# Kernel optimization log

Measured on AMD Instinct MI355X. Metric: run time of the kernel, lower is better.

The kernel has to match this reference:

```python
import jax, jax.numpy as jnp
import numpy as np

N, E = 50000, 800000
IN_CH, OUT_CH, HEADS = 128, 64, 4
NEG_SLOPE = 0.2
BN_EPS = 1e-5


def setup_inputs() -> dict:
    key = jax.random.key(0)
    ks = jax.random.split(key, 8)
    x = jax.random.normal(ks[0], (N, IN_CH), dtype=jnp.float32)
    edge_index = jax.random.randint(ks[1], (2, E), 0, N, dtype=jnp.int64)
    # GATConv params (concat=False: W projects to H*C, output averaged over heads)
    W = jax.random.normal(ks[2], (IN_CH, HEADS * OUT_CH), dtype=jnp.float32) * (1.0 / np.sqrt(IN_CH))
    att_src = jax.random.normal(ks[3], (HEADS, OUT_CH), dtype=jnp.float32) * 0.1
    att_dst = jax.random.normal(ks[4], (HEADS, OUT_CH), dtype=jnp.float32) * 0.1
    bias = jnp.zeros((OUT_CH,), dtype=jnp.float32)
    bn_weight = jnp.ones((OUT_CH,), dtype=jnp.float32)
    bn_bias = jnp.zeros((OUT_CH,), dtype=jnp.float32)
    return {"x": x, "edge_index": edge_index, "W": W, "att_src": att_src,
            "att_dst": att_dst, "bias": bias, "bn_weight": bn_weight, "bn_bias": bn_bias}


def reference(x, edge_index, W, att_src, att_dst, bias, bn_weight, bn_bias):
    # dropout p=0.3 on input and attention weights: identity in eval mode
    n = x.shape[0]
    x_proj = (x @ W).reshape(n, HEADS, OUT_CH)              # [N, H, C]
    a_src = jnp.einsum('nhc,hc->nh', x_proj, att_src)       # [N, H]
    a_dst = jnp.einsum('nhc,hc->nh', x_proj, att_dst)       # [N, H]

    # PyG default add_self_loops=True
    loops = jnp.arange(n, dtype=edge_index.dtype)
    src = jnp.concatenate([edge_index[0], loops])           # [E+N]
    dst = jnp.concatenate([edge_index[1], loops])           # [E+N]

    e = jax.nn.leaky_relu(a_src[src] + a_dst[dst], NEG_SLOPE)  # [E+N, H]
    # edge-softmax per destination node (numerically stable)
    m = jax.ops.segment_max(e, dst, num_segments=n)         # [N, H]
    ex = jnp.exp(e - m[dst])
    denom = jax.ops.segment_sum(ex, dst, num_segments=n)    # [N, H]
    alpha = ex / denom[dst]                                 # [E+N, H]

    msg = alpha[:, :, None] * x_proj[src]                   # [E+N, H, C]
    out = jax.ops.segment_sum(msg, dst, num_segments=n)     # [N, H, C]
    out = out.mean(axis=1) + bias                           # concat=False -> head mean

    # BatchNorm (training-mode batch statistics, biased variance)
    mu = out.mean(axis=0)
    var = out.var(axis=0)
    out = (out - mu) * jax.lax.rsqrt(var + BN_EPS) * bn_weight + bn_bias
    return jax.nn.elu(out)
```

## Files before the change

### kernel.cpp

```cpp
#include <hip/hip_runtime.h>

#define IN_CH 128
#define HC 256
#define OUT_CH 64
#define NEG 0.2f
#define BN_EPS 1e-5f
#define APITCH 136
#define CSR_CAP 4096

typedef __attribute__((ext_vector_type(8))) short short8v;
typedef __attribute__((ext_vector_type(4))) float f32x4v;

__device__ __forceinline__ float4 add4(float4 a, float4 b) {
    return make_float4(a.x + b.x, a.y + b.y, a.z + b.z, a.w + b.w);
}
__device__ __forceinline__ float4 mul4(float4 a, float4 b) {
    return make_float4(a.x * b.x, a.y * b.y, a.z * b.z, a.w * b.w);
}
__device__ __forceinline__ float4 exp4f(float4 a) {
    return make_float4(__expf(a.x), __expf(a.y), __expf(a.z), __expf(a.w));
}
__device__ __forceinline__ float4 leaky4(float4 v) {
    v.x = v.x > 0.f ? v.x : v.x * NEG;
    v.y = v.y > 0.f ? v.y : v.y * NEG;
    v.z = v.z > 0.f ? v.z : v.z * NEG;
    v.w = v.w > 0.f ? v.w : v.w * NEG;
    return v;
}
__device__ __forceinline__ unsigned short f2bf(float f) {
    unsigned u = __float_as_uint(f);
    unsigned r = u + 0x7fffu + ((u >> 16) & 1u);
    return (unsigned short)(r >> 16);
}
__device__ __forceinline__ void acc8(float4& a, float ws, unsigned u) {
    a.x += ws * (float)(u & 0xffu);
    a.y += ws * (float)((u >> 8) & 0xffu);
    a.z += ws * (float)((u >> 16) & 0xffu);
    a.w += ws * (float)(u >> 24);
}

__global__ __launch_bounds__(256) void prep_wt(const float* __restrict__ W,
                                               unsigned short* __restrict__ wt,
                                               unsigned* __restrict__ zeros, int nz) {
    int idx = blockIdx.x * 256 + threadIdx.x;
    if (idx < nz) zeros[idx] = 0u;
    if (idx >= 64 * 64) return;
    int frag = idx >> 6, l = idx & 63;
    int j = frag >> 2, ks = frag & 3;
    int c = l & 15, g = l >> 4;
    int ch = c * 16 + j;
    int k0 = ks * 32 + g * 8;
    unsigned up[4];
    #pragma unroll
    for (int q = 0; q < 4; ++q) {
        unsigned short lo = f2bf(W[(size_t)(k0 + 2 * q) * HC + ch]);
        unsigned short hi = f2bf(W[(size_t)(k0 + 2 * q + 1) * HC + ch]);
        up[q] = (unsigned)lo | ((unsigned)hi << 16);
    }
    *(uint4*)(wt + (size_t)idx * 8) = make_uint4(up[0], up[1], up[2], up[3]);
}

__global__ __launch_bounds__(256) void gemm_and_scatter(const float* __restrict__ x,
                                                        const unsigned short* __restrict__ wt,
                                                        const float* __restrict__ att_src,
                                                        const float* __restrict__ att_dst,
                                                        unsigned char* __restrict__ xq,
                                                        float* __restrict__ pks,
                                                        float* __restrict__ adst, int N,
                                                        const int* __restrict__ ei,
                                                        unsigned* __restrict__ bucket_cnt,
                                                        unsigned* __restrict__ bucketbuf,
                                                        int E, int gemmBlocks) {
    __shared__ unsigned short Al[64][APITCH];
    __shared__ unsigned lcnt[512], lbase[512], lcur[512];
    int t = threadIdx.x;

    if ((int)blockIdx.x >= gemmBlocks) {
        lcnt[t] = 0u; lcnt[t + 256] = 0u;
        lcur[t] = 0u; lcur[t + 256] = 0u;
        __syncthreads();
        int c0 = ((int)blockIdx.x - gemmBlocks) * 4096;
        unsigned rec[16];
        int bk[16];
        #pragma unroll
        for (int i = 0; i < 16; ++i) {
            int e = c0 + t + i * 256;
            bk[i] = -1;
            if (e < E) {
                unsigned s = (unsigned)ei[e];
                unsigned d = (unsigned)ei[E + e];
                rec[i] = s | ((d & 127u) << 16);
                bk[i] = (int)(d >> 7);
                atomicAdd(&lcnt[bk[i]], 1u);
            }
        }
        __syncthreads();
        #pragma unroll
        for (int h = 0; h < 2; ++h) {
            int bi = t + h * 256;
            lbase[bi] = lcnt[bi] ? atomicAdd(&bucket_cnt[bi], lcnt[bi]) : 0u;
        }
        __syncthreads();
        #pragma unroll
        for (int i = 0; i < 16; ++i) {
            if (bk[i] >= 0) {
                unsigned p = lbase[bk[i]] + atomicAdd(&lcur[bk[i]], 1u);
                if (p < CSR_CAP) bucketbuf[(size_t)bk[i] * CSR_CAP + p] = rec[i];
            }
        }
        return;
    }

    int r0 = blockIdx.x * 64;
    #pragma unroll
    for (int i = 0; i < 8; ++i) {
        int f4 = t + i * 256;
        int m = f4 >> 5, kf = f4 & 31;
        float4 v = make_float4(0.f, 0.f, 0.f, 0.f);
        int r = r0 + m;
        if (r < N) v = *(const float4*)(x + (size_t)r * IN_CH + kf * 4);
        ushort4 pk;
        pk.x = f2bf(v.x); pk.y = f2bf(v.y); pk.z = f2bf(v.z); pk.w = f2bf(v.w);
        *(ushort4*)(&Al[m][kf * 4]) = pk;
    }
    __syncthreads();

    int w = t >> 6, l = t & 63;
    int c = l & 15, g = l >> 4;
    int arow = w * 16 + c;

    f32x4v acc[16];
    #pragma unroll
    for (int j = 0; j < 16; ++j) acc[j] = (f32x4v){0.f, 0.f, 0.f, 0.f};

    #pragma unroll
    for (int ks = 0; ks < 4; ++ks) {
        short8v a = *(const short8v*)(&Al[arow][ks * 32 + g * 8]);
        #pragma unroll
        for (int j = 0; j < 16; ++j) {
            short8v b = *(const short8v*)(wt + (size_t)((j * 4 + ks) * 64 + l) * 8);
            acc[j] = __builtin_amdgcn_mfma_f32_16x16x32_bf16(a, b, acc[j], 0, 0, 0);
        }
    }

    float as_c[16], ad_c[16];
    #pragma unroll
    for (int q = 0; q < 4; ++q) {
        *(float4*)(&as_c[q * 4]) = *(const float4*)(att_src + c * 16 + q * 4);
        *(float4*)(&ad_c[q * 4]) = *(const float4*)(att_dst + c * 16 + q * 4);
    }
    #pragma unroll
    for (int i = 0; i < 4; ++i) {
        int r = r0 + w * 16 + g * 4 + i;
        float ps = 0.f, pd = 0.f;
        float amax = 0.f;
        #pragma unroll
        for (int j = 0; j < 16; ++j) {
            float av = acc[j][i];
            ps += av * as_c[j];
            pd += av * ad_c[j];
            amax = fmaxf(amax, fabsf(av));
        }
        ps += __shfl_xor(ps, 1, 64); pd += __shfl_xor(pd, 1, 64);
        ps += __shfl_xor(ps, 2, 64); pd += __shfl_xor(pd, 2, 64);
        amax = fmaxf(amax, __shfl_xor(amax, 1, 64));
        amax = fmaxf(amax, __shfl_xor(amax, 2, 64));
        float inv = amax > 0.f ? 127.f / amax : 0.f;
        if (r < N) {
            int q4 = c & 3, h = c >> 2;
            if (q4 == 0) pks[(size_t)r * 8 + h] = ps;
            else if (q4 == 1) adst[(size_t)r * 4 + h] = pd;
            else if (q4 == 2) pks[(size_t)r * 8 + 4 + h] = amax * (1.f / 127.f);
            unsigned* orow = (unsigned*)(xq + (size_t)r * HC);
            #pragma unroll
            for (int q = 0; q < 4; ++q) {
                unsigned b0 = (unsigned)(int)fmaf(acc[q * 4 + 0][i], inv, 128.5f);
                unsigned b1 = (unsigned)(int)fmaf(acc[q * 4 + 1][i], inv, 128.5f);
                unsigned b2 = (unsigned)(int)fmaf(acc[q * 4 + 2][i], inv, 128.5f);
                unsigned b3 = (unsigned)(int)fmaf(acc[q * 4 + 3][i], inv, 128.5f);
                unsigned pk = b0 | (b1 << 8) | (b2 << 16) | (b3 << 24);
                orow[(((c & 3) * 4 + q) << 2) + h] = pk;
            }
        }
    }
}

__global__ __launch_bounds__(512) void bucket_csr(const unsigned* __restrict__ bucketbuf,
                                                  const unsigned* __restrict__ bucket_cnt,
                                                  unsigned* __restrict__ rowptr,
                                                  unsigned short* __restrict__ ssrc,
                                                  int N, int E, int NB) {
    __shared__ unsigned csum[512];
    __shared__ unsigned dcnt[128], dscan[128], curo[128];
    __shared__ unsigned short sstage[CSR_CAP];
    int b = blockIdx.x, t = threadIdx.x;
    csum[t] = (t < NB) ? bucket_cnt[t] : 0u;
    if (t < 128) dcnt[t] = 0u;
    __syncthreads();
    for (int o = 1; o < 512; o <<= 1) {
        unsigned v = (t >= o) ? csum[t - o] : 0u;
        __syncthreads();
        csum[t] += v;
        __syncthreads();
    }
    unsigned base = (b == 0) ? 0u : csum[b - 1];
    unsigned nloc = bucket_cnt[b];
    if (nloc > CSR_CAP) nloc = CSR_CAP;
    const unsigned* bb = bucketbuf + (size_t)b * CSR_CAP;
    for (unsigned i = t; i < nloc; i += 512) atomicAdd(&dcnt[bb[i] >> 16], 1u);
    __syncthreads();
    if (t < 128) dscan[t] = dcnt[t];
    __syncthreads();
    for (int o = 1; o < 128; o <<= 1) {
        unsigned v = 0u;
        if (t < 128 && t >= o) v = dscan[t - o];
        __syncthreads();
        if (t < 128) dscan[t] += v;
        __syncthreads();
    }
    if (t < 128) {
        unsigned loff = dscan[t] - dcnt[t];
        curo[t] = loff;
        int node = b * 128 + t;
        if (node < N) rowptr[node] = base + loff;
    }
    if (b == 0 && t == 0) rowptr[N] = (unsigned)E;
    __syncthreads();
    for (unsigned i = t; i < nloc; i += 512) {
        unsigned r = bb[i];
        unsigned p = atomicAdd(&curo[r >> 16], 1u);
        sstage[p] = (unsigned short)(r & 0xffffu);
    }
    __syncthreads();
    for (unsigned i = t; i < nloc; i += 512) ssrc[base + i] = sstage[i];
}

__global__ __launch_bounds__(256) void node_fused(const unsigned short* __restrict__ ssrc,
                                                  const unsigned* __restrict__ rowptr,
                                                  const float* __restrict__ pks,
                                                  const float* __restrict__ adst,
                                                  const unsigned char* __restrict__ xq,
                                                  float* __restrict__ out, int N) {
    int wid = (blockIdx.x * 256 + threadIdx.x) >> 6;
    if (wid >= N) return;
    int lane = threadIdx.x & 63;
    int row0 = rowptr[wid];
    int deg = (int)rowptr[wid + 1] - row0;

    float4 ad = *(const float4*)(adst + (size_t)wid * 4);
    float4 saw = *(const float4*)(pks + (size_t)wid * 8);
    float4 scw = *(const float4*)(pks + (size_t)wid * 8 + 4);

    bool isEdge = lane < deg;
    bool active = lane <= deg;
    int s0 = wid;
    float4 as_s = saw, sc_s = scw;
    if (isEdge) {
        s0 = ssrc[row0 + lane];
        as_s = *(const float4*)(pks + (size_t)s0 * 8);
        sc_s = *(const float4*)(pks + (size_t)s0 * 8 + 4);
    }
    float4 ex0 = make_float4(0.f, 0.f, 0.f, 0.f);
    if (active) ex0 = exp4f(leaky4(add4(as_s, ad)));
    float4 sum = ex0;
    if (deg >= 64) {
        for (int j = lane + 64; j < deg; j += 64) {
            int s = ssrc[row0 + j];
            float4 lv = leaky4(add4(*(const float4*)(pks + (size_t)s * 8), ad));
            sum = add4(sum, exp4f(lv));
        }
        if (lane == 63) sum = add4(sum, exp4f(leaky4(add4(saw, ad))));
    }
    #pragma unroll
    for (int m = 1; m < 64; m <<= 1) {
        sum.x += __shfl_xor(sum.x, m, 64);
        sum.y += __shfl_xor(sum.y, m, 64);
        sum.z += __shfl_xor(sum.z, m, 64);
        sum.w += __shfl_xor(sum.w, m, 64);
    }
    float4 inv4 = make_float4(0.25f / sum.x, 0.25f / sum.y, 0.25f / sum.z, 0.25f / sum.w);
    float4 wsv = mul4(mul4(ex0, sc_s), inv4);

    int grp = lane >> 4, sub = lane & 15;
    float4 acc = make_float4(0.f, 0.f, 0.f, 0.f);
    float wssum = 0.f;

    if (deg < 64) {
        int nIter = (deg + 4) >> 2;
        #pragma unroll 4
        for (int it = 0; it < nIter; ++it) {
            int e = it * 4 + grp;
            int s = __shfl(s0, e, 64);
            float w0 = __shfl(wsv.x, e, 64), w1 = __shfl(wsv.y, e, 64);
            float w2 = __shfl(wsv.z, e, 64), w3 = __shfl(wsv.w, e, 64);
            uint4 u = *(const uint4*)(xq + (size_t)s * HC + sub * 16);
            acc8(acc, w0, u.x); acc8(acc, w1, u.y);
            acc8(acc, w2, u.z); acc8(acc, w3, u.w);
            wssum += w0 + w1 + w2 + w3;
        }
    } else {
        float4 selfws = mul4(mul4(exp4f(leaky4(add4(saw, ad))), scw), inv4);
        for (int jb = 0; jb <= deg; jb += 4) {
            int e = jb + grp;
            int ec = e < 64 ? e : 0;
            int s_sh = __shfl(s0, ec, 64);
            float w0 = __shfl(wsv.x, ec, 64), w1 = __shfl(wsv.y, ec, 64);
            float w2 = __shfl(wsv.z, ec, 64), w3 = __shfl(wsv.w, ec, 64);
            int s;
            float4 wv4;
            if (e < deg) {
                if (e < 64) {
                    s = s_sh;
                    wv4 = make_float4(w0, w1, w2, w3);
                } else {
                    s = ssrc[row0 + e];
                    float4 glv = leaky4(add4(*(const float4*)(pks + (size_t)s * 8), ad));
                    float4 gsc = *(const float4*)(pks + (size_t)s * 8 + 4);
                    wv4 = mul4(mul4(exp4f(glv), gsc), inv4);
                }
            } else if (e == deg) {
                s = wid; wv4 = selfws;
            } else {
                s = wid; wv4 = make_float4(0.f, 0.f, 0.f, 0.f);
            }
            uint4 u = *(const uint4*)(xq + (size_t)s * HC + sub * 16);
            acc8(acc, wv4.x, u.x); acc8(acc, wv4.y, u.y);
            acc8(acc, wv4.z, u.z); acc8(acc, wv4.w, u.w);
            wssum += wv4.x + wv4.y + wv4.z + wv4.w;
        }
    }

    #pragma unroll
    for (int m = 16; m < 64; m <<= 1) {
        acc.x += __shfl_xor(acc.x, m, 64);
        acc.y += __shfl_xor(acc.y, m, 64);
        acc.z += __shfl_xor(acc.z, m, 64);
        acc.w += __shfl_xor(acc.w, m, 64);
        wssum += __shfl_xor(wssum, m, 64);
    }
    float off = 128.f * wssum;
    if (lane < 16) {
        float4 o4 = make_float4(acc.x - off, acc.y - off, acc.z - off, acc.w - off);
        *(float4*)(out + (size_t)wid * OUT_CH + sub * 4) = o4;
    }
}

__global__ __launch_bounds__(256) void bn_stats(const float* __restrict__ out,
                                                float* __restrict__ sums,
                                                float* __restrict__ sqs, int N) {
    int c = threadIdx.x & 63, rl = threadIdx.x >> 6;
    float s = 0.f, q = 0.f;
    for (int r = blockIdx.x * 4 + rl; r < N; r += gridDim.x * 4) {
        float v = out[(size_t)r * 64 + c];
        s += v; q += v * v;
    }
    __shared__ float sb[256], qb[256];
    sb[threadIdx.x] = s; qb[threadIdx.x] = q;
    __syncthreads();
    if (rl == 0) {
        s = sb[c] + sb[64 + c] + sb[128 + c] + sb[192 + c];
        q = qb[c] + qb[64 + c] + qb[128 + c] + qb[192 + c];
        atomicAdd(sums + c, s);
        atomicAdd(sqs + c, q);
    }
}

__global__ __launch_bounds__(256) void finalize(float* __restrict__ out,
                                                const float* __restrict__ bnw,
                                                const float* __restrict__ bnb,
                                                const float* __restrict__ sums,
                                                const float* __restrict__ sqs, int N) {
    int idx = blockIdx.x * 256 + threadIdx.x;
    if (idx >= N * 64) return;
    int c = idx & 63;
    float invN = 1.0f / (float)N;
    float mu = sums[c] * invN;
    float var = sqs[c] * invN - mu * mu;
    float v = out[idx];
    float y = (v - mu) * rsqrtf(var + BN_EPS) * bnw[c] + bnb[c];
    out[idx] = y > 0.f ? y : expm1f(y);
}

extern "C" void kernel_launch(void* const* d_in, const int* in_sizes, int n_in,
                              void* d_out, int out_size, void* d_ws, size_t ws_size,
                              hipStream_t stream) {
    const float* x       = (const float*)d_in[0];
    const int*   ei      = (const int*)d_in[1];
    const float* W       = (const float*)d_in[2];
    const float* att_src = (const float*)d_in[3];
    const float* att_dst = (const float*)d_in[4];
    const float* bnw     = (const float*)d_in[6];
    const float* bnb     = (const float*)d_in[7];
    int N = in_sizes[0] / IN_CH;
    int E = in_sizes[1] / 2;
    float* out = (float*)d_out;
    int NB = (N + 127) / 128;

    unsigned char*  xq        = (unsigned char*)d_ws;
    unsigned short* wt        = (unsigned short*)(xq + (size_t)N * HC);
    float*          pks       = (float*)(wt + 64 * 64 * 8);
    float*          adst      = pks + (size_t)N * 8;
    unsigned*       bucket_cnt= (unsigned*)(adst + (size_t)N * 4);
    float*          sums      = (float*)(bucket_cnt + 512);
    float*          sqs       = sums + 64;
    unsigned*       rowptr    = (unsigned*)(sqs + 64);
    unsigned*       bucketbuf = rowptr + N + 1;
    unsigned short* ssrc      = (unsigned short*)(bucketbuf + (size_t)NB * CSR_CAP);

    prep_wt<<<16, 256, 0, stream>>>(W, wt, bucket_cnt, 640);

    int gemmBlocks = (N + 63) / 64;
    int scatBlocks = (E + 4095) / 4096;
    gemm_and_scatter<<<gemmBlocks + scatBlocks, 256, 0, stream>>>(
        x, wt, att_src, att_dst, xq, pks, adst, N, ei, bucket_cnt, bucketbuf, E, gemmBlocks);

    bucket_csr<<<NB, 512, 0, stream>>>(bucketbuf, bucket_cnt, rowptr, ssrc, N, E, NB);

    int gn = (N + 3) / 4;
    node_fused<<<gn, 256, 0, stream>>>(ssrc, rowptr, pks, adst, xq, out, N);

    bn_stats<<<1024, 256, 0, stream>>>(out, sums, sqs, N);
    finalize<<<((N * 64) + 255) / 256, 256, 0, stream>>>(out, bnw, bnb, sums, sqs, N);
}
```

Before: 120.4 us.

## Map each node to a 32-lane half-wave instead of a full wavefront

The node aggregation kernel now gives each destination node 32 lanes instead of 64, so every 64-wide wavefront handles two nodes and the grid shrinks by half. Softmax reductions and the final accumulator reduction use 32-wide shuffles. The gather loop now takes 2 edges per step instead of 4. With about 17 edges per node on average, most lanes of a full wave sat idle, and this mapping is meant to cut that waste. The cost is more loop steps per node and divergence when the two nodes sharing a wave have different degrees.

```diff
diff --git a/kernel.cpp b/kernel.cpp
--- a/kernel.cpp
+++ b/kernel.cpp
@@ -241,9 +241,9 @@
                                                   const float* __restrict__ adst,
                                                   const unsigned char* __restrict__ xq,
                                                   float* __restrict__ out, int N) {
-    int wid = (blockIdx.x * 256 + threadIdx.x) >> 6;
+    int wid = (blockIdx.x * 256 + threadIdx.x) >> 5;
     if (wid >= N) return;
-    int lane = threadIdx.x & 63;
+    int hlane = threadIdx.x & 31;
     int row0 = rowptr[wid];
     int deg = (int)rowptr[wid + 1] - row0;
 
@@ -251,48 +251,50 @@
     float4 saw = *(const float4*)(pks + (size_t)wid * 8);
     float4 scw = *(const float4*)(pks + (size_t)wid * 8 + 4);
 
-    bool isEdge = lane < deg;
-    bool active = lane <= deg;
+    bool isEdge = hlane < deg;
+    bool active = hlane <= deg;
     int s0 = wid;
     float4 as_s = saw, sc_s = scw;
     if (isEdge) {
-        s0 = ssrc[row0 + lane];
+        s0 = ssrc[row0 + hlane];
         as_s = *(const float4*)(pks + (size_t)s0 * 8);
         sc_s = *(const float4*)(pks + (size_t)s0 * 8 + 4);
     }
     float4 ex0 = make_float4(0.f, 0.f, 0.f, 0.f);
-    if (active) ex0 = exp4f(leaky4(add4(as_s, ad)));
+    if (deg < 32 ? active : true) ex0 = exp4f(leaky4(add4(as_s, ad)));
     float4 sum = ex0;
-    if (deg >= 64) {
-        for (int j = lane + 64; j < deg; j += 64) {
+    if (deg >= 32) {
+        for (int j = hlane + 32; j < deg; j += 32) {
             int s = ssrc[row0 + j];
             float4 lv = leaky4(add4(*(const float4*)(pks + (size_t)s * 8), ad));
             sum = add4(sum, exp4f(lv));
         }
-        if (lane == 63) sum = add4(sum, exp4f(leaky4(add4(saw, ad))));
-    }
-    #pragma unroll
-    for (int m = 1; m < 64; m <<= 1) {
-        sum.x += __shfl_xor(sum.x, m, 64);
-        sum.y += __shfl_xor(sum.y, m, 64);
-        sum.z += __shfl_xor(sum.z, m, 64);
-        sum.w += __shfl_xor(sum.w, m, 64);
+        if (hlane == 31) sum = add4(sum, exp4f(leaky4(add4(saw, ad))));
+    }
+    #pragma unroll
+    for (int m = 1; m < 32; m <<= 1) {
+        sum.x += __shfl_xor(sum.x, m, 32);
+        sum.y += __shfl_xor(sum.y, m, 32);
+        sum.z += __shfl_xor(sum.z, m, 32);
+        sum.w += __shfl_xor(sum.w, m, 32);
     }
     float4 inv4 = make_float4(0.25f / sum.x, 0.25f / sum.y, 0.25f / sum.z, 0.25f / sum.w);
     float4 wsv = mul4(mul4(ex0, sc_s), inv4);
 
-    int grp = lane >> 4, sub = lane & 15;
+    int grp = hlane >> 4, sub = hlane & 15;
     float4 acc = make_float4(0.f, 0.f, 0.f, 0.f);
     float wssum = 0.f;
 
-    if (deg < 64) {
-        int nIter = (deg + 4) >> 2;
+    if (deg < 32) {
+        int nIter = (deg + 2) >> 1;
         #pragma unroll 4
         for (int it = 0; it < nIter; ++it) {
-            int e = it * 4 + grp;
-            int s = __shfl(s0, e, 64);
-            float w0 = __shfl(wsv.x, e, 64), w1 = __shfl(wsv.y, e, 64);
-            float w2 = __shfl(wsv.z, e, 64), w3 = __shfl(wsv.w, e, 64);
+            int e = it * 2 + grp;
+            int ec = e < 32 ? e : 0;
+            int s = __shfl(s0, ec, 32);
+            float w0 = __shfl(wsv.x, ec, 32), w1 = __shfl(wsv.y, ec, 32);
+            float w2 = __shfl(wsv.z, ec, 32), w3 = __shfl(wsv.w, ec, 32);
+            if (e >= 32) { w0 = w1 = w2 = w3 = 0.f; s = wid; }
             uint4 u = *(const uint4*)(xq + (size_t)s * HC + sub * 16);
             acc8(acc, w0, u.x); acc8(acc, w1, u.y);
             acc8(acc, w2, u.z); acc8(acc, w3, u.w);
@@ -300,16 +302,16 @@
         }
     } else {
         float4 selfws = mul4(mul4(exp4f(leaky4(add4(saw, ad))), scw), inv4);
-        for (int jb = 0; jb <= deg; jb += 4) {
+        for (int jb = 0; jb <= deg; jb += 2) {
             int e = jb + grp;
-            int ec = e < 64 ? e : 0;
-            int s_sh = __shfl(s0, ec, 64);
-            float w0 = __shfl(wsv.x, ec, 64), w1 = __shfl(wsv.y, ec, 64);
-            float w2 = __shfl(wsv.z, ec, 64), w3 = __shfl(wsv.w, ec, 64);
+            int ec = e < 32 ? e : 0;
+            int s_sh = __shfl(s0, ec, 32);
+            float w0 = __shfl(wsv.x, ec, 32), w1 = __shfl(wsv.y, ec, 32);
+            float w2 = __shfl(wsv.z, ec, 32), w3 = __shfl(wsv.w, ec, 32);
             int s;
             float4 wv4;
             if (e < deg) {
-                if (e < 64) {
+                if (e < 32) {
                     s = s_sh;
                     wv4 = make_float4(w0, w1, w2, w3);
                 } else {
@@ -330,16 +332,13 @@
         }
     }
 
-    #pragma unroll
-    for (int m = 16; m < 64; m <<= 1) {
-        acc.x += __shfl_xor(acc.x, m, 64);
-        acc.y += __shfl_xor(acc.y, m, 64);
-        acc.z += __shfl_xor(acc.z, m, 64);
-        acc.w += __shfl_xor(acc.w, m, 64);
-        wssum += __shfl_xor(wssum, m, 64);
-    }
+    acc.x += __shfl_xor(acc.x, 16, 32);
+    acc.y += __shfl_xor(acc.y, 16, 32);
+    acc.z += __shfl_xor(acc.z, 16, 32);
+    acc.w += __shfl_xor(acc.w, 16, 32);
+    wssum += __shfl_xor(wssum, 16, 32);
     float off = 128.f * wssum;
-    if (lane < 16) {
+    if (hlane < 16) {
         float4 o4 = make_float4(acc.x - off, acc.y - off, acc.z - off, acc.w - off);
         *(float4*)(out + (size_t)wid * OUT_CH + sub * 4) = o4;
     }
@@ -416,7 +415,7 @@
 
     bucket_csr<<<NB, 512, 0, stream>>>(bucketbuf, bucket_cnt, rowptr, ssrc, N, E, NB);
 
-    int gn = (N + 3) / 4;
+    int gn = (N + 7) / 8;
     node_fused<<<gn, 256, 0, stream>>>(ssrc, rowptr, pks, adst, xq, out, N);
 
     bn_stats<<<1024, 256, 0, stream>>>(out, sums, sqs, N);
```

Result: no change. 119.3 us (median of 2 runs) (-0.9%).
